# Kernel optimization log

Measured on AMD Instinct MI355X. Metric: run time of the kernel, lower is better.

The kernel has to match this reference:

```python
import jax, jax.numpy as jnp
import numpy as np

N = 8192
D_IN, D_HID, D_OUT = 64, 128, 64


def setup_inputs() -> dict:
    key = jax.random.key(0)
    ks = jax.random.split(key, 8)
    x = jax.random.normal(ks[0], (N, D_IN), dtype=jnp.float32)
    adj = jax.random.uniform(ks[1], (N, N), dtype=jnp.float32)
    s = 0.05  # small init scale
    W0 = jax.random.normal(ks[2], (D_IN, D_HID), dtype=jnp.float32) * s
    b0 = jnp.zeros((D_HID,), dtype=jnp.float32)
    W1 = jax.random.normal(ks[3], (D_HID, D_HID), dtype=jnp.float32) * s
    b1 = jnp.zeros((D_HID,), dtype=jnp.float32)
    W2 = jax.random.normal(ks[4], (D_HID, D_OUT), dtype=jnp.float32) * s
    b2 = jnp.zeros((D_OUT,), dtype=jnp.float32)
    return {"x": x, "adj": adj, "W0": W0, "b0": b0, "W1": W1, "b1": b1, "W2": W2, "b2": b2}


def laplacian_norm(adj):
    # A_hat = A + I; D^{-1/2} A_hat D^{-1/2}
    A = adj + jnp.eye(adj.shape[0], dtype=adj.dtype)
    dinv = jax.lax.rsqrt(jnp.sum(A, axis=1))
    return A * dinv[:, None] * dinv[None, :]


def reference(x, adj, W0, b0, W1, b1, W2, b2):
    An = laplacian_norm(adj)              # [N, N], computed once, reused per layer
    h = jax.nn.relu(An @ (x @ W0) + b0)   # layer 0 + hidden act
    h = jax.nn.relu(An @ (h @ W1) + b1)   # layer 1 + hidden act
    out = An @ (h @ W2) + b2              # last layer, identity out_act
    return out
```

## Files before the change

kernel.cpp:

```cpp
#include <hip/hip_runtime.h>
#include <type_traits>

typedef unsigned short u16;
typedef unsigned int   u32;
using short8 = __attribute__((ext_vector_type(8))) short;
using f32x4  = __attribute__((ext_vector_type(4))) float;

#define GLD_AS1 const __attribute__((address_space(1))) unsigned
#define GLD_AS3 __attribute__((address_space(3))) unsigned

static constexpr int NN = 8192;

__device__ __forceinline__ u16 f2bf(float f) {
  u32 u = __builtin_bit_cast(u32, f);
  u32 r = (u + 0x7FFFu + ((u >> 16) & 1u)) >> 16;
  return (u16)r;
}
__device__ __forceinline__ float bf2f(u16 h) {
  return __builtin_bit_cast(float, (u32)h << 16);
}
__device__ __forceinline__ short8 cvt8(float4 f0, float4 f1) {
  short8 r;
  r[0] = (short)f2bf(f0.x); r[1] = (short)f2bf(f0.y);
  r[2] = (short)f2bf(f0.z); r[3] = (short)f2bf(f0.w);
  r[4] = (short)f2bf(f1.x); r[5] = (short)f2bf(f1.y);
  r[6] = (short)f2bf(f1.z); r[7] = (short)f2bf(f1.w);
  return r;
}

__global__ __launch_bounds__(256) void rowsum_cvt_k(const float* __restrict__ adj,
                                                    u16* __restrict__ adjb,
                                                    float* __restrict__ dinv) {
  const int row = blockIdx.x;
  const float4* p = (const float4*)(adj + (size_t)row * NN);
  short8* w = (short8*)(adjb + (size_t)row * NN);
  float s = 0.f;
#pragma unroll
  for (int i = 0; i < 4; ++i) {
    const int idx = threadIdx.x + i * 256;
    float4 v0 = p[2 * idx];
    float4 v1 = p[2 * idx + 1];
    s += (v0.x + v0.y) + (v0.z + v0.w) + (v1.x + v1.y) + (v1.z + v1.w);
    w[idx] = cvt8(v0, v1);
  }
#pragma unroll
  for (int off = 32; off > 0; off >>= 1) s += __shfl_down(s, off, 64);
  __shared__ float partial[4];
  if ((threadIdx.x & 63) == 0) partial[threadIdx.x >> 6] = s;
  __syncthreads();
  if (threadIdx.x == 0)
    dinv[row] = rsqrtf(partial[0] + partial[1] + partial[2] + partial[3] + 1.0f);
}

template <typename TIN>
__global__ __launch_bounds__(256) void featmul_k(const TIN* __restrict__ X,
                                                 const float* __restrict__ W,
                                                 const float* __restrict__ dinv,
                                                 u16* __restrict__ Gt,
                                                 u16* __restrict__ U,
                                                 int K, int C) {
  __shared__ __align__(16) u16 Wt[128][128];
  __shared__ float red[4][16][32];
  const int tid = threadIdx.x;
  for (int idx = tid; idx < 128 * 128; idx += 256) {
    int c = idx & 127, k = idx >> 7;
    float w = (k < K && c < C) ? W[k * C + c] : 0.f;
    Wt[c][k] = f2bf(w);
  }
  __syncthreads();
  const int wv = tid >> 6, lane = tid & 63;
  const int q = lane >> 4, m16 = lane & 15;
  const int r0 = blockIdx.x * 16;
  const int c0 = wv * 32;
  f32x4 acc[2];
  acc[0] = {0.f, 0.f, 0.f, 0.f};
  acc[1] = {0.f, 0.f, 0.f, 0.f};
  const TIN* xrow = X + (size_t)(r0 + m16) * K;
  for (int k = 0; k < K; k += 32) {
    short8 af;
    if constexpr (std::is_same_v<TIN, float>) {
      float4 f0 = *(const float4*)(xrow + k + q * 8);
      float4 f1 = *(const float4*)(xrow + k + q * 8 + 4);
      af = cvt8(f0, f1);
    } else {
      af = __builtin_bit_cast(short8, *(const uint4*)(xrow + k + q * 8));
    }
#pragma unroll
    for (int nh = 0; nh < 2; ++nh) {
      short8 bf = *(const short8*)&Wt[c0 + nh * 16 + m16][k + q * 8];
      acc[nh] = __builtin_amdgcn_mfma_f32_16x16x32_bf16(af, bf, acc[nh], 0, 0, 0);
    }
  }
#pragma unroll
  for (int nh = 0; nh < 2; ++nh)
#pragma unroll
    for (int reg = 0; reg < 4; ++reg)
      red[wv][q * 4 + reg][nh * 16 + m16] = acc[nh][reg];
  __syncthreads();
  {
    const int cc = lane & 31, rh = lane >> 5;
    short8 t;
#pragma unroll
    for (int i = 0; i < 8; ++i) {
      int r = rh * 8 + i;
      t[i] = (short)f2bf(red[wv][r][cc] * dinv[r0 + r]);
      U[(size_t)(r0 + r) * 128 + c0 + cc] = (u16)t[i];
    }
    *(uint4*)(Gt + (size_t)(c0 + cc) * NN + r0 + rh * 8) = __builtin_bit_cast(uint4, t);
  }
}

__global__ __launch_bounds__(256, 2) void gcn_gemm(const u16* __restrict__ Adjb,
                                                   const u16* __restrict__ Gt,
                                                   float* __restrict__ P) {
  __shared__ __align__(16) u16 As[2][128 * 64];
  __shared__ __align__(16) u16 Bs[2][128 * 64];

  const int tid = threadIdx.x;
  const int wv = tid >> 6, lane = tid & 63;
  const int wm = wv >> 1, wn = wv & 1;
  const int q = lane >> 4, m16 = lane & 15;
  const int mbase = blockIdx.x * 128;
  const int kbase = blockIdx.y * 1024;
  float* Pt = P + (size_t)blockIdx.y * NN * 128;

  auto stage = [&](int buf, int kc) {
#pragma unroll
    for (int i = 0; i < 4; ++i) {
      const int cl = i * 256 + tid;
      const int r = cl >> 3;
      const int g = (cl & 7) ^ (r & 7);
      const u16* ga = Adjb + (size_t)(mbase + r) * NN + kc + g * 8;
      const u16* gb = Gt + (size_t)r * NN + kc + g * 8;
      __builtin_amdgcn_global_load_lds((GLD_AS1*)ga, (GLD_AS3*)(&As[buf][cl * 8]), 16, 0, 2);
      __builtin_amdgcn_global_load_lds((GLD_AS1*)gb, (GLD_AS3*)(&Bs[buf][cl * 8]), 16, 0, 0);
    }
  };

  f32x4 acc[4][4];
#pragma unroll
  for (int a = 0; a < 4; ++a)
#pragma unroll
    for (int b = 0; b < 4; ++b) acc[a][b] = {0.f, 0.f, 0.f, 0.f};

  stage(0, kbase);
  for (int t = 0; t < 16; ++t) {
    const int buf = t & 1;
    __syncthreads();
    if (t < 15) stage(buf ^ 1, kbase + (t + 1) * 64);
#pragma unroll
    for (int j = 0; j < 2; ++j) {
      short8 af[4], bf[4];
#pragma unroll
      for (int i = 0; i < 4; ++i) {
        const int m = wm * 64 + i * 16 + m16;
        const int n = wn * 64 + i * 16 + m16;
        af[i] = *(const short8*)&As[buf][m * 64 + (((j * 4 + q) ^ (m & 7)) << 3)];
        bf[i] = *(const short8*)&Bs[buf][n * 64 + (((j * 4 + q) ^ (n & 7)) << 3)];
      }
#pragma unroll
      for (int a = 0; a < 4; ++a)
#pragma unroll
        for (int b = 0; b < 4; ++b)
          acc[a][b] = __builtin_amdgcn_mfma_f32_16x16x32_bf16(af[a], bf[b], acc[a][b], 0, 0, 0);
    }
  }

#pragma unroll
  for (int a = 0; a < 4; ++a) {
#pragma unroll
    for (int b = 0; b < 4; ++b) {
      const int c = wn * 64 + b * 16 + m16;
#pragma unroll
      for (int reg = 0; reg < 4; ++reg) {
        const int r = mbase + wm * 64 + a * 16 + q * 4 + reg;
        Pt[(size_t)r * 128 + c] = acc[a][b][reg];
      }
    }
  }
}

template <int RELU, int OUT_F32>
__global__ __launch_bounds__(256) void finalize_k(const float* __restrict__ P,
                                                  const u16* __restrict__ U,
                                                  const float* __restrict__ dinv,
                                                  const float* __restrict__ bias,
                                                  u16* __restrict__ Hout,
                                                  float* __restrict__ Fout) {
  const int tid = threadIdx.x;
  const int c = tid & 127;
  const int r = blockIdx.x * 2 + (tid >> 7);
  const size_t idx = (size_t)r * 128 + c;
  float s = 0.f;
#pragma unroll
  for (int k = 0; k < 8; ++k) s += P[(size_t)k * NN * 128 + idx];
  s += bf2f(U[idx]);
  s = dinv[r] * s + bias[c];
  if (RELU) s = fmaxf(s, 0.f);
  if (OUT_F32) {
    if (c < 64) Fout[(size_t)r * 64 + c] = s;
  } else {
    Hout[idx] = f2bf(s);
  }
}

extern "C" void kernel_launch(void* const* d_in, const int* in_sizes, int n_in,
                              void* d_out, int out_size, void* d_ws, size_t ws_size,
                              hipStream_t stream) {
  const float* x   = (const float*)d_in[0];
  const float* adj = (const float*)d_in[1];
  const float* W0  = (const float*)d_in[2];
  const float* b0  = (const float*)d_in[3];
  const float* W1  = (const float*)d_in[4];
  const float* b1  = (const float*)d_in[5];
  const float* W2  = (const float*)d_in[6];
  const float* b2  = (const float*)d_in[7];
  float* out = (float*)d_out;

  char* ws = (char*)d_ws;
  float* dinv = (float*)ws;
  u16* Gt     = (u16*)(ws + (1u << 20));
  u16* U      = (u16*)(ws + (4u << 20));
  u16* h      = (u16*)(ws + (6u << 20));
  float* Pp   = (float*)(ws + (8u << 20));
  u16* adjb   = (u16*)(ws + (48u << 20));

  const dim3 ggrid(64, 8);

  rowsum_cvt_k<<<NN, 256, 0, stream>>>(adj, adjb, dinv);

  featmul_k<float><<<NN / 16, 256, 0, stream>>>(x, W0, dinv, Gt, U, 64, 128);
  gcn_gemm<<<ggrid, 256, 0, stream>>>(adjb, Gt, Pp);
  finalize_k<1, 0><<<NN / 2, 256, 0, stream>>>(Pp, U, dinv, b0, h, nullptr);

  featmul_k<u16><<<NN / 16, 256, 0, stream>>>(h, W1, dinv, Gt, U, 128, 128);
  gcn_gemm<<<ggrid, 256, 0, stream>>>(adjb, Gt, Pp);
  finalize_k<1, 0><<<NN / 2, 256, 0, stream>>>(Pp, U, dinv, b1, h, nullptr);

  featmul_k<u16><<<NN / 16, 256, 0, stream>>>(h, W2, dinv, Gt, U, 128, 64);
  gcn_gemm<<<ggrid, 256, 0, stream>>>(adjb, Gt, Pp);
  finalize_k<0, 1><<<NN / 2, 256, 0, stream>>>(Pp, U, dinv, b2, nullptr, out);
}
```

Baseline: 602.6 us.

## Triple-buffer GCN GEMM with 256-row tiles, 512 threads and vmcnt waits

The aggregation GEMM moves from 128-row to 256-row M tiles with 8 waves per block and halves the grid along M. The double-buffered LDS pipeline becomes three stages: two tiles are prefetched up front, and each step waits on vmcnt instead of a full __syncthreads, so global-to-LDS loads overlap compute more deeply. Global load offsets are now computed once outside the K loop. The A-tile load cache hint is dropped, and the fp32 adjacency read in the rowsum kernel switches to nontemporal loads. The larger LDS footprint (about 147 KB) likely limits occupancy to one block per CU, trading occupancy for reuse of the B tile.

```diff
diff --git a/kernel.cpp b/kernel.cpp
--- a/kernel.cpp
+++ b/kernel.cpp
@@ -19,12 +19,13 @@
 __device__ __forceinline__ float bf2f(u16 h) {
   return __builtin_bit_cast(float, (u32)h << 16);
 }
-__device__ __forceinline__ short8 cvt8(float4 f0, float4 f1) {
+__device__ __forceinline__ short8 cvt8(f32x4 f0, f32x4 f1) {
   short8 r;
-  r[0] = (short)f2bf(f0.x); r[1] = (short)f2bf(f0.y);
-  r[2] = (short)f2bf(f0.z); r[3] = (short)f2bf(f0.w);
-  r[4] = (short)f2bf(f1.x); r[5] = (short)f2bf(f1.y);
-  r[6] = (short)f2bf(f1.z); r[7] = (short)f2bf(f1.w);
+#pragma unroll
+  for (int i = 0; i < 4; ++i) {
+    r[i]     = (short)f2bf(f0[i]);
+    r[4 + i] = (short)f2bf(f1[i]);
+  }
   return r;
 }
 
@@ -32,15 +33,15 @@
                                                     u16* __restrict__ adjb,
                                                     float* __restrict__ dinv) {
   const int row = blockIdx.x;
-  const float4* p = (const float4*)(adj + (size_t)row * NN);
+  const f32x4* p = (const f32x4*)(adj + (size_t)row * NN);
   short8* w = (short8*)(adjb + (size_t)row * NN);
   float s = 0.f;
 #pragma unroll
   for (int i = 0; i < 4; ++i) {
     const int idx = threadIdx.x + i * 256;
-    float4 v0 = p[2 * idx];
-    float4 v1 = p[2 * idx + 1];
-    s += (v0.x + v0.y) + (v0.z + v0.w) + (v1.x + v1.y) + (v1.z + v1.w);
+    f32x4 v0 = __builtin_nontemporal_load(p + 2 * idx);
+    f32x4 v1 = __builtin_nontemporal_load(p + 2 * idx + 1);
+    s += (v0[0] + v0[1]) + (v0[2] + v0[3]) + (v1[0] + v1[1]) + (v1[2] + v1[3]);
     w[idx] = cvt8(v0, v1);
   }
 #pragma unroll
@@ -79,8 +80,8 @@
   for (int k = 0; k < K; k += 32) {
     short8 af;
     if constexpr (std::is_same_v<TIN, float>) {
-      float4 f0 = *(const float4*)(xrow + k + q * 8);
-      float4 f1 = *(const float4*)(xrow + k + q * 8 + 4);
+      f32x4 f0 = *(const f32x4*)(xrow + k + q * 8);
+      f32x4 f1 = *(const f32x4*)(xrow + k + q * 8 + 4);
       af = cvt8(f0, f1);
     } else {
       af = __builtin_bit_cast(short8, *(const uint4*)(xrow + k + q * 8));
@@ -110,31 +111,50 @@
   }
 }
 
-__global__ __launch_bounds__(256, 2) void gcn_gemm(const u16* __restrict__ Adjb,
+__global__ __launch_bounds__(512, 2) void gcn_gemm(const u16* __restrict__ Adjb,
                                                    const u16* __restrict__ Gt,
                                                    float* __restrict__ P) {
-  __shared__ __align__(16) u16 As[2][128 * 64];
-  __shared__ __align__(16) u16 Bs[2][128 * 64];
+  __shared__ __align__(16) u16 As[3][256 * 64];
+  __shared__ __align__(16) u16 Bs[3][128 * 64];
 
   const int tid = threadIdx.x;
   const int wv = tid >> 6, lane = tid & 63;
   const int wm = wv >> 1, wn = wv & 1;
   const int q = lane >> 4, m16 = lane & 15;
-  const int mbase = blockIdx.x * 128;
+  const int mbase = blockIdx.x * 256;
   const int kbase = blockIdx.y * 1024;
   float* Pt = P + (size_t)blockIdx.y * NN * 128;
 
+  size_t aoff[4];
+  int acl[4];
+  size_t boff[2];
+  int bcl[2];
+#pragma unroll
+  for (int i = 0; i < 4; ++i) {
+    const int cl = i * 512 + tid;
+    const int r = cl >> 3;
+    const int g = (cl & 7) ^ (r & 7);
+    aoff[i] = (size_t)(mbase + r) * NN + g * 8;
+    acl[i] = cl;
+  }
+#pragma unroll
+  for (int i = 0; i < 2; ++i) {
+    const int cl = i * 512 + tid;
+    const int r = cl >> 3;
+    const int g = (cl & 7) ^ (r & 7);
+    boff[i] = (size_t)r * NN + g * 8;
+    bcl[i] = cl;
+  }
+
   auto stage = [&](int buf, int kc) {
 #pragma unroll
-    for (int i = 0; i < 4; ++i) {
-      const int cl = i * 256 + tid;
-      const int r = cl >> 3;
-      const int g = (cl & 7) ^ (r & 7);
-      const u16* ga = Adjb + (size_t)(mbase + r) * NN + kc + g * 8;
-      const u16* gb = Gt + (size_t)r * NN + kc + g * 8;
-      __builtin_amdgcn_global_load_lds((GLD_AS1*)ga, (GLD_AS3*)(&As[buf][cl * 8]), 16, 0, 2);
-      __builtin_amdgcn_global_load_lds((GLD_AS1*)gb, (GLD_AS3*)(&Bs[buf][cl * 8]), 16, 0, 0);
-    }
+    for (int i = 0; i < 4; ++i)
+      __builtin_amdgcn_global_load_lds((GLD_AS1*)(Adjb + aoff[i] + kc),
+                                       (GLD_AS3*)(&As[buf][acl[i] * 8]), 16, 0, 0);
+#pragma unroll
+    for (int i = 0; i < 2; ++i)
+      __builtin_amdgcn_global_load_lds((GLD_AS1*)(Gt + boff[i] + kc),
+                                       (GLD_AS3*)(&Bs[buf][bcl[i] * 8]), 16, 0, 0);
   };
 
   f32x4 acc[4][4];
@@ -144,10 +164,17 @@
     for (int b = 0; b < 4; ++b) acc[a][b] = {0.f, 0.f, 0.f, 0.f};
 
   stage(0, kbase);
+  stage(1, kbase + 64);
   for (int t = 0; t < 16; ++t) {
-    const int buf = t & 1;
-    __syncthreads();
-    if (t < 15) stage(buf ^ 1, kbase + (t + 1) * 64);
+    const int buf = t % 3;
+    if (t < 15) {
+      asm volatile("s_waitcnt vmcnt(6)" ::: "memory");
+    } else {
+      asm volatile("s_waitcnt vmcnt(0)" ::: "memory");
+    }
+    __builtin_amdgcn_s_barrier();
+    asm volatile("" ::: "memory");
+    if (t + 2 < 16) stage((t + 2) % 3, kbase + (t + 2) * 64);
 #pragma unroll
     for (int j = 0; j < 2; ++j) {
       short8 af[4], bf[4];
@@ -225,19 +252,19 @@
   float* Pp   = (float*)(ws + (8u << 20));
   u16* adjb   = (u16*)(ws + (48u << 20));
 
-  const dim3 ggrid(64, 8);
+  const dim3 ggrid(32, 8);
 
   rowsum_cvt_k<<<NN, 256, 0, stream>>>(adj, adjb, dinv);
 
   featmul_k<float><<<NN / 16, 256, 0, stream>>>(x, W0, dinv, Gt, U, 64, 128);
-  gcn_gemm<<<ggrid, 256, 0, stream>>>(adjb, Gt, Pp);
+  gcn_gemm<<<ggrid, 512, 0, stream>>>(adjb, Gt, Pp);
   finalize_k<1, 0><<<NN / 2, 256, 0, stream>>>(Pp, U, dinv, b0, h, nullptr);
 
   featmul_k<u16><<<NN / 16, 256, 0, stream>>>(h, W1, dinv, Gt, U, 128, 128);
-  gcn_gemm<<<ggrid, 256, 0, stream>>>(adjb, Gt, Pp);
+  gcn_gemm<<<ggrid, 512, 0, stream>>>(adjb, Gt, Pp);
   finalize_k<1, 0><<<NN / 2, 256, 0, stream>>>(Pp, U, dinv, b1, h, nullptr);
 
   featmul_k<u16><<<NN / 16, 256, 0, stream>>>(h, W2, dinv, Gt, U, 128, 64);
-  gcn_gemm<<<ggrid, 256, 0, stream>>>(adjb, Gt, Pp);
+  gcn_gemm<<<ggrid, 512, 0, stream>>>(adjb, Gt, Pp);
   finalize_k<0, 1><<<NN / 2, 256, 0, stream>>>(Pp, U, dinv, b2, nullptr, out);
 }
```

New measurement: 572.8 us. -4.9%, faster.
